# Performance work log

Measured on AMD Instinct MI355X. Metric: run time of the kernel, lower is better.

Reference implementation:

```python
import jax, jax.numpy as jnp
import numpy as np

BLOCK_SIZE = 256
N_EMBED = 384
HEAD_SIZE = 64


def setup_inputs() -> dict:
    key = jax.random.key(0)
    kx, kq, kk, kv = jax.random.split(key, 4)
    B, T = 256, 256
    x = jax.random.normal(kx, (B, T, N_EMBED), dtype=jnp.float32)
    # nn.Linear(n_embed, head_size, bias=False): y = x @ W.T with W [head, embed].
    # We store the transposed weight [embed, head] so forward is x @ W.
    scale = 1.0 / np.sqrt(N_EMBED)
    Wq = jax.random.normal(kq, (N_EMBED, HEAD_SIZE), dtype=jnp.float32) * scale
    Wk = jax.random.normal(kk, (N_EMBED, HEAD_SIZE), dtype=jnp.float32) * scale
    Wv = jax.random.normal(kv, (N_EMBED, HEAD_SIZE), dtype=jnp.float32) * scale
    return {"x": x, "Wq": Wq, "Wk": Wk, "Wv": Wv}


def reference(x, Wq, Wk, Wv):
    B, T, C = x.shape  # C == N_EMBED
    q = jnp.einsum('btc,ch->bth', x, Wq)
    k = jnp.einsum('btc,ch->bth', x, Wk)
    v = jnp.einsum('btc,ch->bth', x, Wv)
    # NOTE: original scales by 1/sqrt(C) where C = embed dim (384), not head_size.
    wei = jnp.einsum('bth,bsh->bts', q, k) / jnp.sqrt(jnp.float32(C))
    causal = jnp.tril(jnp.ones((T, T), dtype=bool))
    wei = jnp.where(causal, wei, -jnp.inf)
    wei = jax.nn.softmax(wei, axis=-1)
    # dropout is identity in eval mode (reference is deterministic)
    out = jnp.einsum('bts,bsh->bth', wei, v)
    return out
```

## Files before the change

### kernel.cpp

```cpp
#include <hip/hip_runtime.h>


typedef short s16x8 __attribute__((ext_vector_type(8)));
typedef float f32x4 __attribute__((ext_vector_type(4)));

#define MFMA16(a, b, c) __builtin_amdgcn_mfma_f32_16x16x32_bf16((a), (b), (c), 0, 0, 0)

__device__ __forceinline__ unsigned short f2bf(float f) {
  unsigned u = __builtin_bit_cast(unsigned, f);
  u += 0x7fffu + ((u >> 16) & 1u);
  return (unsigned short)(u >> 16);
}
__device__ __forceinline__ unsigned pack2(float lo, float hi) {
  return (unsigned)f2bf(lo) | ((unsigned)f2bf(hi) << 16);
}

__global__ __launch_bounds__(256) void wcvt(
    const float* __restrict__ Wq, const float* __restrict__ Wk,
    const float* __restrict__ Wv, unsigned short* __restrict__ Wt_sw) {
  int idx = blockIdx.x * 256 + threadIdx.x;
  int j = idx & 7;
  int c = idx >> 3;
  int n15 = c & 15;
  int q4 = (c >> 4) & 3;
  int g = c >> 6;
  int nt = g % 12;
  int kc = g / 12;
  int n = nt * 16 + n15;
  int kk = kc * 32 + q4 * 8 + j;
  const float* src = (n < 64) ? Wq : (n < 128) ? Wk : Wv;
  float v = src[kk * 64 + (n & 63)];
  if (n < 64) v *= 0.05103103630798287f;
  Wt_sw[idx] = f2bf(v);
}

__global__ __launch_bounds__(256, 2) void qkv_proj(
    const float* __restrict__ x, const unsigned short* __restrict__ Wt_sw,
    unsigned short* __restrict__ q_sw, unsigned short* __restrict__ k_sw,
    unsigned short* __restrict__ v_sw) {
  const int tid = threadIdx.x;
  const int lane = tid & 63;
  const int wv = tid >> 6;
  const int n15 = lane & 15;
  const int q4 = lane >> 4;
  const long row0 = (long)blockIdx.x * 128 + wv * 32;

  f32x4 acc[12][2];
#pragma unroll
  for (int i = 0; i < 12; ++i)
#pragma unroll
    for (int t = 0; t < 2; ++t) acc[i][t] = (f32x4){0.f, 0.f, 0.f, 0.f};

  const float* xp0 = x + (row0 + n15) * 384 + q4 * 8;
  const float* xp1 = x + (row0 + 16 + n15) * 384 + q4 * 8;
  float4 c00 = *reinterpret_cast<const float4*>(xp0);
  float4 c01 = *reinterpret_cast<const float4*>(xp0 + 4);
  float4 c10 = *reinterpret_cast<const float4*>(xp1);
  float4 c11 = *reinterpret_cast<const float4*>(xp1 + 4);

  s16x8 wc[12];
#pragma unroll
  for (int nt = 0; nt < 12; ++nt)
    wc[nt] = *reinterpret_cast<const s16x8*>(Wt_sw + nt * 512 + lane * 8);

  for (int kc = 0; kc < 12; ++kc) {
    const int nkc = (kc < 11) ? kc + 1 : 11;
    float4 p00 = *reinterpret_cast<const float4*>(xp0 + nkc * 32);
    float4 p01 = *reinterpret_cast<const float4*>(xp0 + nkc * 32 + 4);
    float4 p10 = *reinterpret_cast<const float4*>(xp1 + nkc * 32);
    float4 p11 = *reinterpret_cast<const float4*>(xp1 + nkc * 32 + 4);
    s16x8 wn[12];
#pragma unroll
    for (int nt = 0; nt < 12; ++nt)
      wn[nt] = *reinterpret_cast<const s16x8*>(Wt_sw + (nkc * 12 + nt) * 512 + lane * 8);

    s16x8 xa[2];
    xa[0][0] = (short)f2bf(c00.x); xa[0][1] = (short)f2bf(c00.y);
    xa[0][2] = (short)f2bf(c00.z); xa[0][3] = (short)f2bf(c00.w);
    xa[0][4] = (short)f2bf(c01.x); xa[0][5] = (short)f2bf(c01.y);
    xa[0][6] = (short)f2bf(c01.z); xa[0][7] = (short)f2bf(c01.w);
    xa[1][0] = (short)f2bf(c10.x); xa[1][1] = (short)f2bf(c10.y);
    xa[1][2] = (short)f2bf(c10.z); xa[1][3] = (short)f2bf(c10.w);
    xa[1][4] = (short)f2bf(c11.x); xa[1][5] = (short)f2bf(c11.y);
    xa[1][6] = (short)f2bf(c11.z); xa[1][7] = (short)f2bf(c11.w);

#pragma unroll
    for (int nt = 0; nt < 12; ++nt) {
#pragma unroll
      for (int t = 0; t < 2; ++t) {
        if (nt < 8) acc[nt][t] = MFMA16(wc[nt], xa[t], acc[nt][t]);
        else        acc[nt][t] = MFMA16(xa[t], wc[nt], acc[nt][t]);
      }
    }
    c00 = p00; c01 = p01; c10 = p10; c11 = p11;
#pragma unroll
    for (int nt = 0; nt < 12; ++nt) wc[nt] = wn[nt];
  }

  const long bb_ = row0 >> 8;
  unsigned short* qb = q_sw + bb_ * 16384;
  unsigned short* kb = k_sw + bb_ * 16384;
  unsigned short* vb = v_sw + bb_ * 16384;
#pragma unroll
  for (int t = 0; t < 2; ++t) {
    const int rb = (int)(row0 & 255) + t * 16;
    const int qtile = rb >> 4;
#pragma unroll
    for (int mt = 0; mt < 4; ++mt) {
      const int off = ((qtile * 2 + (mt >> 1)) * 64 + (2 * (mt & 1) + (q4 >> 1)) * 16 + n15) * 8
                      + (q4 & 1) * 4;
      uint2 sq, sk;
      sq.x = pack2(acc[mt][t][0], acc[mt][t][1]);
      sq.y = pack2(acc[mt][t][2], acc[mt][t][3]);
      sk.x = pack2(acc[4 + mt][t][0], acc[4 + mt][t][1]);
      sk.y = pack2(acc[4 + mt][t][2], acc[4 + mt][t][3]);
      *reinterpret_cast<uint2*>(qb + off) = sq;
      *reinterpret_cast<uint2*>(kb + off) = sk;
    }
    const int s0 = rb + q4 * 4;
#pragma unroll
    for (int nt = 0; nt < 4; ++nt) {
      const int off = (((s0 >> 5) * 4 + nt) * 64 + ((s0 >> 3) & 3) * 16 + n15) * 8 + (s0 & 7);
      uint2 sv;
      sv.x = pack2(acc[8 + nt][t][0], acc[8 + nt][t][1]);
      sv.y = pack2(acc[8 + nt][t][2], acc[8 + nt][t][3]);
      *reinterpret_cast<uint2*>(vb + off) = sv;
    }
  }
}

__global__ __launch_bounds__(256) void attn(
    const unsigned short* __restrict__ q_sw, const unsigned short* __restrict__ k_sw,
    const unsigned short* __restrict__ v_sw, float* __restrict__ out) {
  __shared__ unsigned short Ps[4][16 * 264];
  const int b = blockIdx.x & 255;
  const int j = blockIdx.x >> 8;
  const int tid = threadIdx.x;
  const int wv = tid >> 6;
  const int lane = tid & 63;
  const int n15 = lane & 15;
  const int q4 = lane >> 4;

  const int qt = (wv == 0) ? j : (wv == 1) ? 7 - j : (wv == 2) ? 8 + j : 15 - j;

  unsigned short* pbuf = &Ps[wv][0];
  if (!(qt & 1)) {
    int r = lane >> 2, c = lane & 3;
    *reinterpret_cast<uint2*>(pbuf + r * 264 + (qt + 1) * 16 + c * 4) = make_uint2(0u, 0u);
  }

  const unsigned short* qb = q_sw + b * 16384;
  const unsigned short* kb = k_sw + b * 16384;
  const unsigned short* vb = v_sw + b * 16384;

  const s16x8 qf0 = *reinterpret_cast<const s16x8*>(qb + (qt * 2 + 0) * 512 + lane * 8);
  const s16x8 qf1 = *reinterpret_cast<const s16x8*>(qb + (qt * 2 + 1) * 512 + lane * 8);

  float sm[4] = {0.f, 0.f, 0.f, 0.f};
  s16x8 kf0 = *reinterpret_cast<const s16x8*>(kb + 0 * 512 + lane * 8);
  s16x8 kf1 = *reinterpret_cast<const s16x8*>(kb + 1 * 512 + lane * 8);
#pragma unroll 16
  for (int ct = 0; ct < 16; ++ct) {
    if (ct > qt) break;
    const int nc = (ct < qt) ? ct + 1 : ct;
    s16x8 nf0 = *reinterpret_cast<const s16x8*>(kb + (nc * 2 + 0) * 512 + lane * 8);
    s16x8 nf1 = *reinterpret_cast<const s16x8*>(kb + (nc * 2 + 1) * 512 + lane * 8);
    f32x4 a = (f32x4){0.f, 0.f, 0.f, 0.f};
    a = MFMA16(qf0, kf0, a);
    a = MFMA16(qf1, kf1, a);
    const bool diag = (ct == qt);
#pragma unroll
    for (int e = 0; e < 4; ++e) {
      float p = (diag && (n15 > q4 * 4 + e)) ? 0.f : __expf(a[e]);
      sm[e] += p;
      pbuf[(q4 * 4 + e) * 264 + ct * 16 + n15] = f2bf(p);
    }
    kf0 = nf0; kf1 = nf1;
  }
#pragma unroll
  for (int off = 1; off < 16; off <<= 1)
#pragma unroll
    for (int e = 0; e < 4; ++e) sm[e] += __shfl_xor(sm[e], off);
  float rn[4];
#pragma unroll
  for (int e = 0; e < 4; ++e) rn[e] = 1.0f / sm[e];

  f32x4 O[4];
#pragma unroll
  for (int nt = 0; nt < 4; ++nt) O[nt] = (f32x4){0.f, 0.f, 0.f, 0.f};
  const int nk = (qt + 2) >> 1;
  s16x8 vf[4], vn[4];
#pragma unroll
  for (int nt = 0; nt < 4; ++nt)
    vf[nt] = *reinterpret_cast<const s16x8*>(vb + nt * 512 + lane * 8);
#pragma unroll 8
  for (int kc = 0; kc < 8; ++kc) {
    if (kc >= nk) break;
    const int ncc = (kc + 1 < nk) ? kc + 1 : kc;
#pragma unroll
    for (int nt = 0; nt < 4; ++nt)
      vn[nt] = *reinterpret_cast<const s16x8*>(vb + (ncc * 4 + nt) * 512 + lane * 8);
    s16x8 pf = *reinterpret_cast<const s16x8*>(pbuf + n15 * 264 + kc * 32 + q4 * 8);
#pragma unroll
    for (int nt = 0; nt < 4; ++nt) {
      O[nt] = MFMA16(pf, vf[nt], O[nt]);
      vf[nt] = vn[nt];
    }
  }
#pragma unroll
  for (int nt = 0; nt < 4; ++nt)
#pragma unroll
    for (int e = 0; e < 4; ++e)
      out[(size_t)(b * 256 + qt * 16 + q4 * 4 + e) * 64 + nt * 16 + n15] = O[nt][e] * rn[e];
}

extern "C" void kernel_launch(void* const* d_in, const int* in_sizes, int n_in,
                              void* d_out, int out_size, void* d_ws, size_t ws_size,
                              hipStream_t stream) {
  const float* x  = (const float*)d_in[0];
  const float* Wq = (const float*)d_in[1];
  const float* Wk = (const float*)d_in[2];
  const float* Wv = (const float*)d_in[3];
  float* out = (float*)d_out;

  unsigned short* q_sw = (unsigned short*)d_ws;
  unsigned short* k_sw = q_sw + (size_t)65536 * 64;
  unsigned short* v_sw = k_sw + (size_t)65536 * 64;
  unsigned short* Wt_sw = v_sw + (size_t)65536 * 64;

  wcvt<<<288, 256, 0, stream>>>(Wq, Wk, Wv, Wt_sw);
  qkv_proj<<<512, 256, 0, stream>>>(x, Wt_sw, q_sw, k_sw, v_sw);
  attn<<<1024, 256, 0, stream>>>(q_sw, k_sw, v_sw, out);
}
```

Baseline: 179.6 us.

## Keep attention probabilities in registers via transposed QK^T and lane shuffles

The attention kernel now computes S^T by swapping the MFMA operands, so each lane holds probabilities for one query column across keys. It packs them into registers and rebuilds the A-operand for the PV MFMA with cross-lane shuffles instead of staging through shared memory. The row-sum reduction shrinks to two shuffles plus a final broadcast. Separately, the manual bf16 rounding is replaced by native bf16 conversion intrinsics. This removes LDS traffic and the scalar 16-bit stores, at the cost of many more shuffles per PV step and 16 packed register slots.

```diff
diff --git a/kernel.cpp b/kernel.cpp
--- a/kernel.cpp
+++ b/kernel.cpp
@@ -3,16 +3,25 @@
 
 typedef short s16x8 __attribute__((ext_vector_type(8)));
 typedef float f32x4 __attribute__((ext_vector_type(4)));
+typedef float f32x2 __attribute__((ext_vector_type(2)));
+typedef unsigned u32x4 __attribute__((ext_vector_type(4)));
+typedef __bf16 bf16x2t __attribute__((ext_vector_type(2)));
 
 #define MFMA16(a, b, c) __builtin_amdgcn_mfma_f32_16x16x32_bf16((a), (b), (c), 0, 0, 0)
 
 __device__ __forceinline__ unsigned short f2bf(float f) {
-  unsigned u = __builtin_bit_cast(unsigned, f);
-  u += 0x7fffu + ((u >> 16) & 1u);
-  return (unsigned short)(u >> 16);
-}
-__device__ __forceinline__ unsigned pack2(float lo, float hi) {
-  return (unsigned)f2bf(lo) | ((unsigned)f2bf(hi) << 16);
+  return __builtin_bit_cast(unsigned short, (__bf16)f);
+}
+__device__ __forceinline__ unsigned cvt2(float a, float b) {
+  f32x2 t; t[0] = a; t[1] = b;
+  bf16x2t r = __builtin_convertvector(t, bf16x2t);
+  return __builtin_bit_cast(unsigned, r);
+}
+__device__ __forceinline__ s16x8 cvt8(float4 a, float4 b) {
+  u32x4 u;
+  u[0] = cvt2(a.x, a.y); u[1] = cvt2(a.z, a.w);
+  u[2] = cvt2(b.x, b.y); u[3] = cvt2(b.z, b.w);
+  return __builtin_bit_cast(s16x8, u);
 }
 
 __global__ __launch_bounds__(256) void wcvt(
@@ -75,14 +84,8 @@
       wn[nt] = *reinterpret_cast<const s16x8*>(Wt_sw + (nkc * 12 + nt) * 512 + lane * 8);
 
     s16x8 xa[2];
-    xa[0][0] = (short)f2bf(c00.x); xa[0][1] = (short)f2bf(c00.y);
-    xa[0][2] = (short)f2bf(c00.z); xa[0][3] = (short)f2bf(c00.w);
-    xa[0][4] = (short)f2bf(c01.x); xa[0][5] = (short)f2bf(c01.y);
-    xa[0][6] = (short)f2bf(c01.z); xa[0][7] = (short)f2bf(c01.w);
-    xa[1][0] = (short)f2bf(c10.x); xa[1][1] = (short)f2bf(c10.y);
-    xa[1][2] = (short)f2bf(c10.z); xa[1][3] = (short)f2bf(c10.w);
-    xa[1][4] = (short)f2bf(c11.x); xa[1][5] = (short)f2bf(c11.y);
-    xa[1][6] = (short)f2bf(c11.z); xa[1][7] = (short)f2bf(c11.w);
+    xa[0] = cvt8(c00, c01);
+    xa[1] = cvt8(c10, c11);
 
 #pragma unroll
     for (int nt = 0; nt < 12; ++nt) {
@@ -110,10 +113,10 @@
       const int off = ((qtile * 2 + (mt >> 1)) * 64 + (2 * (mt & 1) + (q4 >> 1)) * 16 + n15) * 8
                       + (q4 & 1) * 4;
       uint2 sq, sk;
-      sq.x = pack2(acc[mt][t][0], acc[mt][t][1]);
-      sq.y = pack2(acc[mt][t][2], acc[mt][t][3]);
-      sk.x = pack2(acc[4 + mt][t][0], acc[4 + mt][t][1]);
-      sk.y = pack2(acc[4 + mt][t][2], acc[4 + mt][t][3]);
+      sq.x = cvt2(acc[mt][t][0], acc[mt][t][1]);
+      sq.y = cvt2(acc[mt][t][2], acc[mt][t][3]);
+      sk.x = cvt2(acc[4 + mt][t][0], acc[4 + mt][t][1]);
+      sk.y = cvt2(acc[4 + mt][t][2], acc[4 + mt][t][3]);
       *reinterpret_cast<uint2*>(qb + off) = sq;
       *reinterpret_cast<uint2*>(kb + off) = sk;
     }
@@ -122,8 +125,8 @@
     for (int nt = 0; nt < 4; ++nt) {
       const int off = (((s0 >> 5) * 4 + nt) * 64 + ((s0 >> 3) & 3) * 16 + n15) * 8 + (s0 & 7);
       uint2 sv;
-      sv.x = pack2(acc[8 + nt][t][0], acc[8 + nt][t][1]);
-      sv.y = pack2(acc[8 + nt][t][2], acc[8 + nt][t][3]);
+      sv.x = cvt2(acc[8 + nt][t][0], acc[8 + nt][t][1]);
+      sv.y = cvt2(acc[8 + nt][t][2], acc[8 + nt][t][3]);
       *reinterpret_cast<uint2*>(vb + off) = sv;
     }
   }
@@ -132,7 +135,6 @@
 __global__ __launch_bounds__(256) void attn(
     const unsigned short* __restrict__ q_sw, const unsigned short* __restrict__ k_sw,
     const unsigned short* __restrict__ v_sw, float* __restrict__ out) {
-  __shared__ unsigned short Ps[4][16 * 264];
   const int b = blockIdx.x & 255;
   const int j = blockIdx.x >> 8;
   const int tid = threadIdx.x;
@@ -143,12 +145,6 @@
 
   const int qt = (wv == 0) ? j : (wv == 1) ? 7 - j : (wv == 2) ? 8 + j : 15 - j;
 
-  unsigned short* pbuf = &Ps[wv][0];
-  if (!(qt & 1)) {
-    int r = lane >> 2, c = lane & 3;
-    *reinterpret_cast<uint2*>(pbuf + r * 264 + (qt + 1) * 16 + c * 4) = make_uint2(0u, 0u);
-  }
-
   const unsigned short* qb = q_sw + b * 16384;
   const unsigned short* kb = k_sw + b * 16384;
   const unsigned short* vb = v_sw + b * 16384;
@@ -156,7 +152,8 @@
   const s16x8 qf0 = *reinterpret_cast<const s16x8*>(qb + (qt * 2 + 0) * 512 + lane * 8);
   const s16x8 qf1 = *reinterpret_cast<const s16x8*>(qb + (qt * 2 + 1) * 512 + lane * 8);
 
-  float sm[4] = {0.f, 0.f, 0.f, 0.f};
+  uint2 pk[16];
+  float psum = 0.f;
   s16x8 kf0 = *reinterpret_cast<const s16x8*>(kb + 0 * 512 + lane * 8);
   s16x8 kf1 = *reinterpret_cast<const s16x8*>(kb + 1 * 512 + lane * 8);
 #pragma unroll 16
@@ -166,24 +163,22 @@
     s16x8 nf0 = *reinterpret_cast<const s16x8*>(kb + (nc * 2 + 0) * 512 + lane * 8);
     s16x8 nf1 = *reinterpret_cast<const s16x8*>(kb + (nc * 2 + 1) * 512 + lane * 8);
     f32x4 a = (f32x4){0.f, 0.f, 0.f, 0.f};
-    a = MFMA16(qf0, kf0, a);
-    a = MFMA16(qf1, kf1, a);
+    a = MFMA16(kf0, qf0, a);
+    a = MFMA16(kf1, qf1, a);
     const bool diag = (ct == qt);
+    float p[4];
 #pragma unroll
     for (int e = 0; e < 4; ++e) {
-      float p = (diag && (n15 > q4 * 4 + e)) ? 0.f : __expf(a[e]);
-      sm[e] += p;
-      pbuf[(q4 * 4 + e) * 264 + ct * 16 + n15] = f2bf(p);
-    }
+      p[e] = (diag && (q4 * 4 + e > n15)) ? 0.f : __expf(a[e]);
+      psum += p[e];
+    }
+    pk[ct].x = cvt2(p[0], p[1]);
+    pk[ct].y = cvt2(p[2], p[3]);
     kf0 = nf0; kf1 = nf1;
   }
-#pragma unroll
-  for (int off = 1; off < 16; off <<= 1)
-#pragma unroll
-    for (int e = 0; e < 4; ++e) sm[e] += __shfl_xor(sm[e], off);
-  float rn[4];
-#pragma unroll
-  for (int e = 0; e < 4; ++e) rn[e] = 1.0f / sm[e];
+  psum += __shfl_xor(psum, 16);
+  psum += __shfl_xor(psum, 32);
+  const float rn_col = 1.0f / psum;
 
   f32x4 O[4];
 #pragma unroll
@@ -193,6 +188,8 @@
 #pragma unroll
   for (int nt = 0; nt < 4; ++nt)
     vf[nt] = *reinterpret_cast<const s16x8*>(vb + nt * 512 + lane * 8);
+  const int laneA = ((q4 & 1) << 5) + n15;
+  const bool hi = (q4 >> 1) != 0;
 #pragma unroll 8
   for (int kc = 0; kc < 8; ++kc) {
     if (kc >= nk) break;
@@ -200,18 +197,30 @@
 #pragma unroll
     for (int nt = 0; nt < 4; ++nt)
       vn[nt] = *reinterpret_cast<const s16x8*>(vb + (ncc * 4 + nt) * 512 + lane * 8);
-    s16x8 pf = *reinterpret_cast<const s16x8*>(pbuf + n15 * 264 + kc * 32 + q4 * 8);
+    const uint2 t0 = pk[2 * kc];
+    const uint2 t1 = (2 * kc + 1 <= qt) ? pk[2 * kc + 1] : make_uint2(0u, 0u);
+    unsigned r0a = __shfl(t0.x, laneA),      r0b = __shfl(t0.y, laneA);
+    unsigned r0c = __shfl(t0.x, laneA + 16), r0d = __shfl(t0.y, laneA + 16);
+    unsigned r1a = __shfl(t1.x, laneA),      r1b = __shfl(t1.y, laneA);
+    unsigned r1c = __shfl(t1.x, laneA + 16), r1d = __shfl(t1.y, laneA + 16);
+    u32x4 u;
+    u[0] = hi ? r1a : r0a; u[1] = hi ? r1b : r0b;
+    u[2] = hi ? r1c : r0c; u[3] = hi ? r1d : r0d;
+    s16x8 pf = __builtin_bit_cast(s16x8, u);
 #pragma unroll
     for (int nt = 0; nt < 4; ++nt) {
       O[nt] = MFMA16(pf, vf[nt], O[nt]);
       vf[nt] = vn[nt];
     }
   }
+  float rnm[4];
+#pragma unroll
+  for (int e = 0; e < 4; ++e) rnm[e] = __shfl(rn_col, q4 * 4 + e);
 #pragma unroll
   for (int nt = 0; nt < 4; ++nt)
 #pragma unroll
     for (int e = 0; e < 4; ++e)
-      out[(size_t)(b * 256 + qt * 16 + q4 * 4 + e) * 64 + nt * 16 + n15] = O[nt][e] * rn[e];
+      out[(size_t)(b * 256 + qt * 16 + q4 * 4 + e) * 64 + nt * 16 + n15] = O[nt][e] * rnm[e];
 }
 
 extern "C" void kernel_launch(void* const* d_in, const int* in_sizes, int n_in,
```

Measured after the change: 201.6 us. 1.12x slower.
